# Kernel optimization log

Measured on AMD Instinct MI355X. Metric: run time of the kernel, lower is better.

Reference implementation:

```python
import jax, jax.numpy as jnp
import numpy as np

N, E, D, L, G, C = 20000, 320000, 512, 6, 64, 10
EPS = 1e-5


def setup_inputs() -> dict:
    key = jax.random.key(0)
    ks = jax.random.split(key, 8)
    s = 0.05  # small init scale to keep activations sane across 6 layers
    x = jax.random.normal(ks[0], (N, D), jnp.float32)
    edge_index = jax.random.randint(ks[1], (2, E), 0, N, jnp.int32)
    batch = jnp.sort(jax.random.randint(ks[2], (N,), 0, G, jnp.int32))
    W_rel = jax.random.normal(ks[3], (L, D, D), jnp.float32) * s
    b_rel = jnp.zeros((L, D), jnp.float32)
    W_root = jax.random.normal(ks[4], (L, D, D), jnp.float32) * s
    gamma = jnp.ones((L, D), jnp.float32)
    beta = jnp.zeros((L, D), jnp.float32)
    lin_w = jax.random.normal(ks[5], (D, C), jnp.float32) * s
    lin_b = jnp.zeros((C,), jnp.float32)
    return {"x": x, "edge_index": edge_index, "batch": batch,
            "W_rel": W_rel, "b_rel": b_rel, "W_root": W_root,
            "gamma": gamma, "beta": beta, "lin_w": lin_w, "lin_b": lin_b}


def reference(x, edge_index, batch, W_rel, b_rel, W_root, gamma, beta, lin_w, lin_b):
    # PyG GraphConv (aggr='add'): out = segment_sum(x[src] -> dst) @ W_rel + b_rel + x @ W_root
    src, dst = edge_index[0], edge_index[1]
    n = x.shape[0]
    for l in range(W_rel.shape[0]):  # 6 structurally identical layers
        agg = jax.ops.segment_sum(x[src], dst, num_segments=n)  # [N, D]
        h = agg @ W_rel[l] + b_rel[l] + x @ W_root[l]
        # BatchNorm1d in training mode: biased batch statistics over nodes
        mu = jnp.mean(h, axis=0)
        var = jnp.mean(jnp.square(h - mu), axis=0)
        x = jax.nn.relu((h - mu) * jax.lax.rsqrt(var + EPS) * gamma[l] + beta[l])
    # global_mean_pool over per-node graph ids
    sums = jax.ops.segment_sum(x, batch, num_segments=G)              # [G, D]
    counts = jax.ops.segment_sum(jnp.ones((n,), x.dtype), batch, num_segments=G)
    pooled = sums / jnp.maximum(counts, 1.0)[:, None]
    return pooled @ lin_w + lin_b  # [G, C]
```

## Files before the change

### kernel.cpp

```cpp
#include <hip/hip_runtime.h>


typedef unsigned short u16;
typedef unsigned int u32;
typedef __attribute__((ext_vector_type(8))) short bf16x8;
typedef __attribute__((ext_vector_type(16))) float f32x16;
typedef __attribute__((ext_vector_type(2))) float f32x2;

#define DFEAT 512
#define KDIM 1024
#define NLAYER 6
#define NGRAPH 64
#define NCLS 10
#define BN_EPS 1e-5f
#define NBUCKET 1024

__device__ __forceinline__ float bf_lo(u32 u) { union { u32 i; float f; } v; v.i = u << 16; return v.f; }
__device__ __forceinline__ float bf_hi(u32 u) { union { u32 i; float f; } v; v.i = u & 0xFFFF0000u; return v.f; }
__device__ __forceinline__ u16 f2bf(float f) {
  union { float f; u32 i; } v; v.f = f;
  u32 r = v.i + 0x7FFFu + ((v.i >> 16) & 1u);
  return (u16)(r >> 16);
}
__device__ __forceinline__ u32 pack2(float lo, float hi) {
  return (u32)f2bf(lo) | ((u32)f2bf(hi) << 16);
}

__device__ __forceinline__ void gload_lds16(const u16* g, u16* lds_base) {
  __builtin_amdgcn_global_load_lds(
      (const __attribute__((address_space(1))) u32*)g,
      (__attribute__((address_space(3))) u32*)lds_base, 16, 0, 0);
}

__global__ void prep_kernel(const int* __restrict__ ei, int* __restrict__ counts, int E,
                            const float* __restrict__ Wrel, const float* __restrict__ Wroot,
                            u16* __restrict__ Wt,
                            const float* __restrict__ x, u16* __restrict__ A, int M,
                            int histB, int wB) {
  __shared__ float tile[64][65];
  int b = blockIdx.x;
  int tid = threadIdx.x;
  if (b < histB) {
    int e = b * 256 + tid;
    if (e < E) atomicAdd(&counts[ei[E + e]], 1);
  } else if (b < histB + wB) {
    int t = b - histB;
    int l = t >> 7;
    int tt = t & 127;
    int k0 = (tt >> 3) << 6;
    int n0 = (tt & 7) << 6;
    int rr = tid >> 4;
    int c4 = (tid & 15) << 2;
#pragma unroll
    for (int i = 0; i < 4; i++) {
      int k = k0 + i * 16 + rr;
      const float* src = (k < DFEAT)
          ? &Wrel[((size_t)l * DFEAT + k) * DFEAT + n0 + c4]
          : &Wroot[((size_t)l * DFEAT + (k - DFEAT)) * DFEAT + n0 + c4];
      float4 v = *(const float4*)src;
      float* d = &tile[i * 16 + rr][c4];
      d[0] = v.x; d[1] = v.y; d[2] = v.z; d[3] = v.w;
    }
    __syncthreads();
    int nr = tid >> 3;
    int kc = (tid & 7) << 3;
#pragma unroll
    for (int i = 0; i < 2; i++) {
      int nl = i * 32 + nr;
      uint4 o;
      o.x = pack2(tile[kc + 0][nl], tile[kc + 1][nl]);
      o.y = pack2(tile[kc + 2][nl], tile[kc + 3][nl]);
      o.z = pack2(tile[kc + 4][nl], tile[kc + 5][nl]);
      o.w = pack2(tile[kc + 6][nl], tile[kc + 7][nl]);
      *(uint4*)&Wt[(size_t)(l * DFEAT + n0 + nl) * KDIM + k0 + kc] = o;
    }
  } else {
    int idx = (b - histB - wB) * 256 + tid;
    int row = idx >> 7;
    int c4 = (idx & 127) * 4;
    if (row < M) {
      float4 v = *(const float4*)&x[(size_t)row * DFEAT + c4];
      uint2 o; o.x = pack2(v.x, v.y); o.y = pack2(v.z, v.w);
      *(uint2*)&A[(size_t)row * KDIM + DFEAT + c4] = o;
    }
  }
}

__global__ __launch_bounds__(1024) void dscan_kernel(const int* __restrict__ counts,
                                                     int* __restrict__ base0,
                                                     int* __restrict__ bcur,
                                                     int* __restrict__ edgebase,
                                                     int* __restrict__ row_ptr2, int n) {
  __shared__ int hist[NBUCKET];
  __shared__ int part[NBUCKET];
  int tid = threadIdx.x;
  hist[tid] = 0;
  __syncthreads();
  for (int i = tid; i < n; i += 1024) {
    int d = counts[i]; if (d > NBUCKET - 1) d = NBUCKET - 1;
    atomicAdd(&hist[d], 1);
  }
  __syncthreads();
  int c = hist[tid];
  part[tid] = c; __syncthreads();
  int x = c;
  for (int off = 1; off < NBUCKET; off <<= 1) {
    int t = (tid >= off) ? part[tid - off] : 0;
    __syncthreads();
    x += t; part[tid] = x;
    __syncthreads();
  }
  base0[tid] = x - c;
  bcur[tid] = x - c;
  int w = c * tid;
  part[tid] = w; __syncthreads();
  int y = w;
  for (int off = 1; off < NBUCKET; off <<= 1) {
    int t = (tid >= off) ? part[tid - off] : 0;
    __syncthreads();
    y += t; part[tid] = y;
    __syncthreads();
  }
  edgebase[tid] = y - w;
  if (tid == NBUCKET - 1) row_ptr2[n] = y;
}

__global__ __launch_bounds__(256) void rank_kernel(const int* __restrict__ counts,
                                                   const int* __restrict__ base0,
                                                   int* __restrict__ bcur,
                                                   const int* __restrict__ edgebase,
                                                   int* __restrict__ perm,
                                                   int* __restrict__ row_ptr2,
                                                   int* __restrict__ cursor2, int n) {
  __shared__ int hb[NBUCKET];
  __shared__ int hstart[NBUCKET];
  int tid = threadIdx.x;
  for (int d = tid; d < NBUCKET; d += 256) hb[d] = 0;
  __syncthreads();
  int row = blockIdx.x * 256 + tid;
  bool valid = (row < n);
  int deg = 0, j = 0;
  if (valid) {
    deg = counts[row]; if (deg > NBUCKET - 1) deg = NBUCKET - 1;
    j = atomicAdd(&hb[deg], 1);
  }
  __syncthreads();
  for (int d = tid; d < NBUCKET; d += 256) {
    int c = hb[d];
    hstart[d] = c ? atomicAdd(&bcur[d], c) : 0;
  }
  __syncthreads();
  if (valid) {
    int rnk = hstart[deg] + j;
    int jj = rnk - base0[deg];
    int v = edgebase[deg] + jj * deg;
    perm[rnk] = row;
    row_ptr2[rnk] = v;
    cursor2[row] = v;
  }
}

__global__ void scatter_kernel(const int* __restrict__ ei, int* __restrict__ cursor2,
                               int* __restrict__ csr2, int E) {
  int e = blockIdx.x * 256 + threadIdx.x;
  if (e < E) {
    int d = ei[E + e];
    int pos = atomicAdd(&cursor2[d], 1);
    csr2[pos] = ei[e];
  }
}

template <bool FUSED>
__device__ __forceinline__ void acc8(uint4 v, const f32x2* sc, const f32x2* sh, f32x2* a) {
  f32x2 t0 = {bf_lo(v.x), bf_hi(v.x)};
  f32x2 t1 = {bf_lo(v.y), bf_hi(v.y)};
  f32x2 t2 = {bf_lo(v.z), bf_hi(v.z)};
  f32x2 t3 = {bf_lo(v.w), bf_hi(v.w)};
  if constexpr (FUSED) {
    f32x2 z = {0.f, 0.f};
    a[0] += __builtin_elementwise_max(t0 * sc[0] + sh[0], z);
    a[1] += __builtin_elementwise_max(t1 * sc[1] + sh[1], z);
    a[2] += __builtin_elementwise_max(t2 * sc[2] + sh[2], z);
    a[3] += __builtin_elementwise_max(t3 * sc[3] + sh[3], z);
  } else {
    a[0] += t0; a[1] += t1; a[2] += t2; a[3] += t3;
  }
}

#define GCAP 1536
template <bool FUSED>
__global__ __launch_bounds__(256) void gather_kernel(u16* __restrict__ A,
                                                     const u16* __restrict__ Hb,
                                                     const float* __restrict__ sums,
                                                     const float* __restrict__ gamma,
                                                     const float* __restrict__ beta,
                                                     const int* __restrict__ row_ptr2,
                                                     const int* __restrict__ csr2,
                                                     const int* __restrict__ perm,
                                                     int n, float invN) {
  __shared__ int sidx[GCAP];
  int b = blockIdx.x;
  int slice = b & 7;
  int grp = b >> 3;
  int tid = threadIdx.x;
  int r0 = grp * 32;
  int rend = (r0 + 32 < n) ? (r0 + 32) : n;
  int wbeg = row_ptr2[r0], wend = row_ptr2[rend];
  int cnt = wend - wbeg;
  bool lds_ok = (cnt <= GCAP);
  if (lds_ok)
    for (int t = tid; t < cnt; t += 256) sidx[t] = csr2[wbeg + t];
  __syncthreads();

  int wid = tid >> 6, lane = tid & 63;
  int dsub = lane >> 3, fl = lane & 7;
  int rnk = r0 + wid * 8 + dsub;
  if (rnk >= n) return;
  int dst = perm[rnk];
  int cc = slice * 64 + fl * 8;
  f32x2 sc2[4], sh2[4];
  if constexpr (FUSED) {
#pragma unroll
    for (int j = 0; j < 8; j++) {
      int c = cc + j;
      float mu = sums[c] * invN;
      float var = sums[DFEAT + c] * invN - mu * mu;
      float s = gamma[c] * rsqrtf(var + BN_EPS);
      sc2[j >> 1][j & 1] = s;
      sh2[j >> 1][j & 1] = beta[c] - mu * s;
    }
    uint4 h = *(const uint4*)&Hb[(size_t)dst * DFEAT + cc];
    f32x2 z = {0.f, 0.f};
    f32x2 e0 = __builtin_elementwise_max((f32x2){bf_lo(h.x), bf_hi(h.x)} * sc2[0] + sh2[0], z);
    f32x2 e1 = __builtin_elementwise_max((f32x2){bf_lo(h.y), bf_hi(h.y)} * sc2[1] + sh2[1], z);
    f32x2 e2 = __builtin_elementwise_max((f32x2){bf_lo(h.z), bf_hi(h.z)} * sc2[2] + sh2[2], z);
    f32x2 e3 = __builtin_elementwise_max((f32x2){bf_lo(h.w), bf_hi(h.w)} * sc2[3] + sh2[3], z);
    uint4 o;
    o.x = pack2(e0[0], e0[1]); o.y = pack2(e1[0], e1[1]);
    o.z = pack2(e2[0], e2[1]); o.w = pack2(e3[0], e3[1]);
    *(uint4*)&A[(size_t)dst * KDIM + DFEAT + cc] = o;
  }
  const u16* Sx = FUSED ? (Hb + cc) : (A + DFEAT + cc);
  const size_t RS = FUSED ? DFEAT : KDIM;
  int db = row_ptr2[rnk], de = row_ptr2[rnk + 1];
  f32x2 a[4] = {};
  if (lds_ok) {
    int e = db - wbeg, ee = de - wbeg;
    for (; e + 7 < ee; e += 8) {
      int s0 = sidx[e + 0], s1 = sidx[e + 1], s2 = sidx[e + 2], s3 = sidx[e + 3];
      int s4 = sidx[e + 4], s5 = sidx[e + 5], s6 = sidx[e + 6], s7 = sidx[e + 7];
      uint4 v0 = *(const uint4*)&Sx[(size_t)s0 * RS];
      uint4 v1 = *(const uint4*)&Sx[(size_t)s1 * RS];
      uint4 v2 = *(const uint4*)&Sx[(size_t)s2 * RS];
      uint4 v3 = *(const uint4*)&Sx[(size_t)s3 * RS];
      uint4 v4 = *(const uint4*)&Sx[(size_t)s4 * RS];
      uint4 v5 = *(const uint4*)&Sx[(size_t)s5 * RS];
      uint4 v6 = *(const uint4*)&Sx[(size_t)s6 * RS];
      uint4 v7 = *(const uint4*)&Sx[(size_t)s7 * RS];
      acc8<FUSED>(v0, sc2, sh2, a); acc8<FUSED>(v1, sc2, sh2, a);
      acc8<FUSED>(v2, sc2, sh2, a); acc8<FUSED>(v3, sc2, sh2, a);
      acc8<FUSED>(v4, sc2, sh2, a); acc8<FUSED>(v5, sc2, sh2, a);
      acc8<FUSED>(v6, sc2, sh2, a); acc8<FUSED>(v7, sc2, sh2, a);
    }
    for (; e < ee; ++e) {
      uint4 v = *(const uint4*)&Sx[(size_t)sidx[e] * RS];
      acc8<FUSED>(v, sc2, sh2, a);
    }
  } else {
    for (int e = db; e < de; ++e) {
      uint4 v = *(const uint4*)&Sx[(size_t)csr2[e] * RS];
      acc8<FUSED>(v, sc2, sh2, a);
    }
  }
  uint4 o;
  o.x = pack2(a[0][0], a[0][1]); o.y = pack2(a[1][0], a[1][1]);
  o.z = pack2(a[2][0], a[2][1]); o.w = pack2(a[3][0], a[3][1]);
  *(uint4*)&A[(size_t)dst * KDIM + cc] = o;
}

#define BM 128
#define BN 128
#define BK 64
#define CSTR 132
__global__ __launch_bounds__(256, 4) void gemm_kernel(const u16* __restrict__ A,
                                                      const u16* __restrict__ Bt,
                                                      const float* __restrict__ bias,
                                                      u16* __restrict__ Hb,
                                                      float* __restrict__ sums, int M) {
  const int lin = blockIdx.x;
  const int bx = ((lin >> 5) << 3) + (lin & 7);
  const int by = (lin >> 3) & 3;
  const int m0 = bx * BM;
  if (m0 >= M) return;
  const int n0 = by * BN;

  __shared__ u16 smem[BM * CSTR];
  __shared__ float sred[2 * BN];
  u16* As = smem;
  u16* Bs = smem + BM * BK;
  const int tid = threadIdx.x;
  const int wid = tid >> 6, lane = tid & 63;
  const int wm = wid >> 1, wn = wid & 1;
  const int l31 = lane & 31, half = lane >> 5;

  if (tid < 2 * BN) sred[tid] = 0.f;

  const int dr = lane >> 3;
  const int gcol = ((lane & 7) ^ dr) * 8;
  int arow[4], brow[4];
#pragma unroll
  for (int t = 0; t < 4; t++) {
    int r = wid * 32 + t * 8 + dr;
    int ar = m0 + r; if (ar >= M) ar = M - 1;
    arow[t] = ar;
    brow[t] = n0 + r;
  }

  f32x16 acc[2][2] = {};

  for (int k0 = 0; k0 < KDIM; k0 += BK) {
    __syncthreads();
#pragma unroll
    for (int t = 0; t < 4; t++)
      gload_lds16(&A[(size_t)arow[t] * KDIM + k0 + gcol], &As[(wid * 32 + t * 8) * BK]);
#pragma unroll
    for (int t = 0; t < 4; t++)
      gload_lds16(&Bt[(size_t)brow[t] * KDIM + k0 + gcol], &Bs[(wid * 32 + t * 8) * BK]);
    __syncthreads();
#pragma unroll
    for (int ks = 0; ks < 4; ks++) {
      int slot = ((ks * 2 + half) ^ (l31 & 7)) * 8;
      bf16x8 a0 = *(const bf16x8*)&As[(wm * 64 + l31) * BK + slot];
      bf16x8 a1 = *(const bf16x8*)&As[(wm * 64 + 32 + l31) * BK + slot];
      bf16x8 b0 = *(const bf16x8*)&Bs[(wn * 64 + l31) * BK + slot];
      bf16x8 b1 = *(const bf16x8*)&Bs[(wn * 64 + 32 + l31) * BK + slot];
      acc[0][0] = __builtin_amdgcn_mfma_f32_32x32x16_bf16(a0, b0, acc[0][0], 0, 0, 0);
      acc[0][1] = __builtin_amdgcn_mfma_f32_32x32x16_bf16(a0, b1, acc[0][1], 0, 0, 0);
      acc[1][0] = __builtin_amdgcn_mfma_f32_32x32x16_bf16(a1, b0, acc[1][0], 0, 0, 0);
      acc[1][1] = __builtin_amdgcn_mfma_f32_32x32x16_bf16(a1, b1, acc[1][1], 0, 0, 0);
    }
  }

  __syncthreads();

#pragma unroll
  for (int nt = 0; nt < 2; nt++) {
    int colt = wn * 64 + nt * 32 + l31;
    float bv = bias[n0 + colt];
    float s = 0.f, s2 = 0.f;
#pragma unroll
    for (int mt = 0; mt < 2; mt++) {
      int rbase = wm * 64 + mt * 32 + half * 4;
#pragma unroll
      for (int reg = 0; reg < 16; reg++) {
        int rowt = rbase + (reg & 3) + 8 * (reg >> 2);
        float v = acc[mt][nt][reg] + bv;
        smem[rowt * CSTR + colt] = f2bf(v);
        if (m0 + rowt < M) { s += v; s2 += v * v; }
      }
    }
    s  += __shfl_xor(s, 32);
    s2 += __shfl_xor(s2, 32);
    if (half == 0) {
      atomicAdd(&sred[colt], s);
      atomicAdd(&sred[BN + colt], s2);
    }
  }
  __syncthreads();

  const int rsub = tid >> 4;
  const int c8 = (tid & 15) * 8;
#pragma unroll
  for (int it = 0; it < 8; it++) {
    int rowt = it * 16 + rsub;
    int grow = m0 + rowt;
    if (grow < M) {
      uint4 v = *(const uint4*)&smem[rowt * CSTR + c8];
      *(uint4*)&Hb[(size_t)grow * DFEAT + n0 + c8] = v;
    }
  }
  if (tid < BN) {
    atomicAdd(&sums[n0 + tid], sred[tid]);
    atomicAdd(&sums[DFEAT + n0 + tid], sred[BN + tid]);
  }
}

__device__ __forceinline__ int lower_bound_dev(const int* a, int n, int v) {
  int lo = 0, hi = n;
  while (lo < hi) { int mid = (lo + hi) >> 1; if (a[mid] < v) lo = mid + 1; else hi = mid; }
  return lo;
}

__global__ __launch_bounds__(1024) void pool_kernel(const u16* __restrict__ Hb,
                                                    const float* __restrict__ sums,
                                                    const float* __restrict__ gamma,
                                                    const float* __restrict__ beta,
                                                    const int* __restrict__ batch,
                                                    float* __restrict__ pooled, int n, float invN) {
  __shared__ float red[DFEAT];
  int g = blockIdx.x;
  int tid = threadIdx.x;
  if (tid < DFEAT) red[tid] = 0.f;
  int lo = lower_bound_dev(batch, n, g);
  int hi = lower_bound_dev(batch, n, g + 1);
  int rowOff = tid >> 6, lane = tid & 63;
  int c0 = lane * 8;
  float sc[8], sh[8];
#pragma unroll
  for (int j = 0; j < 8; j++) {
    int c = c0 + j;
    float mu = sums[c] * invN;
    float var = sums[DFEAT + c] * invN - mu * mu;
    float s = gamma[c] * rsqrtf(var + BN_EPS);
    sc[j] = s;
    sh[j] = beta[c] - mu * s;
  }
  float a[8] = {};
  for (int r = lo + rowOff; r < hi; r += 16) {
    uint4 v = *(const uint4*)&Hb[(size_t)r * DFEAT + c0];
    float e0 = bf_lo(v.x), e1 = bf_hi(v.x), e2 = bf_lo(v.y), e3 = bf_hi(v.y);
    float e4 = bf_lo(v.z), e5 = bf_hi(v.z), e6 = bf_lo(v.w), e7 = bf_hi(v.w);
    a[0] += fmaxf(e0 * sc[0] + sh[0], 0.f); a[1] += fmaxf(e1 * sc[1] + sh[1], 0.f);
    a[2] += fmaxf(e2 * sc[2] + sh[2], 0.f); a[3] += fmaxf(e3 * sc[3] + sh[3], 0.f);
    a[4] += fmaxf(e4 * sc[4] + sh[4], 0.f); a[5] += fmaxf(e5 * sc[5] + sh[5], 0.f);
    a[6] += fmaxf(e6 * sc[6] + sh[6], 0.f); a[7] += fmaxf(e7 * sc[7] + sh[7], 0.f);
  }
  __syncthreads();
#pragma unroll
  for (int j = 0; j < 8; j++) atomicAdd(&red[c0 + j], a[j]);
  __syncthreads();
  if (tid < DFEAT) pooled[g * DFEAT + tid] = red[tid] / fmaxf((float)(hi - lo), 1.0f);
}

__global__ __launch_bounds__(64) void final_kernel(const float* __restrict__ pooled,
                                                   const float* __restrict__ lin_w,
                                                   const float* __restrict__ lin_b,
                                                   float* __restrict__ out) {
  int g = blockIdx.x;
  int lane = threadIdx.x;
  float acc[NCLS] = {};
  float4 p0 = *(const float4*)&pooled[g * DFEAT + lane * 8];
  float4 p1 = *(const float4*)&pooled[g * DFEAT + lane * 8 + 4];
  float pv[8] = {p0.x, p0.y, p0.z, p0.w, p1.x, p1.y, p1.z, p1.w};
#pragma unroll
  for (int j = 0; j < 8; j++) {
    int k = lane * 8 + j;
#pragma unroll
    for (int c = 0; c < NCLS; c++) acc[c] += pv[j] * lin_w[k * NCLS + c];
  }
#pragma unroll
  for (int off = 32; off > 0; off >>= 1)
#pragma unroll
    for (int c = 0; c < NCLS; c++) acc[c] += __shfl_down(acc[c], off);
  if (lane == 0)
#pragma unroll
    for (int c = 0; c < NCLS; c++) out[g * NCLS + c] = acc[c] + lin_b[c];
}

extern "C" void kernel_launch(void* const* d_in, const int* in_sizes, int n_in,
                              void* d_out, int out_size, void* d_ws, size_t ws_size,
                              hipStream_t stream) {
  const float* x      = (const float*)d_in[0];
  const int*   ei     = (const int*)d_in[1];
  const int*   batch  = (const int*)d_in[2];
  const float* W_rel  = (const float*)d_in[3];
  const float* b_rel  = (const float*)d_in[4];
  const float* W_root = (const float*)d_in[5];
  const float* gamma  = (const float*)d_in[6];
  const float* beta   = (const float*)d_in[7];
  const float* lin_w  = (const float*)d_in[8];
  const float* lin_b  = (const float*)d_in[9];
  float* out = (float*)d_out;

  const int N = in_sizes[0] / DFEAT;
  const int E = in_sizes[1] / 2;

  char* p = (char*)d_ws;
  u16*   A        = (u16*)p;    p += (size_t)N * KDIM * 2;
  u16*   Hb       = (u16*)p;    p += (size_t)N * DFEAT * 2;
  u16*   Wt       = (u16*)p;    p += (size_t)NLAYER * DFEAT * KDIM * 2;
  int*   row_ptr2 = (int*)p;    p += ((size_t)(N + 1) * 4 + 15) / 16 * 16;
  int*   counts   = (int*)p;    p += (size_t)N * 4;
  int*   cursor2  = (int*)p;    p += (size_t)N * 4;
  int*   perm     = (int*)p;    p += (size_t)N * 4;
  int*   csr2     = (int*)p;    p += (size_t)E * 4;
  int*   base0    = (int*)p;    p += (size_t)NBUCKET * 4;
  int*   bcur     = (int*)p;    p += (size_t)NBUCKET * 4;
  int*   edgebase = (int*)p;    p += (size_t)NBUCKET * 4;
  float* sums     = (float*)p;  p += (size_t)NLAYER * 2 * DFEAT * 4;
  float* pooled   = (float*)p;  p += (size_t)NGRAPH * DFEAT * 4;

  const float invN = 1.0f / (float)N;

  hipMemsetAsync(counts, 0, (size_t)N * 4, stream);
  hipMemsetAsync(sums, 0, (size_t)NLAYER * 2 * DFEAT * 4, stream);

  const int histB = (E + 255) / 256;
  const int wB = NLAYER * 128;
  const int xB = (N * 128 + 255) / 256;
  prep_kernel<<<histB + wB + xB, 256, 0, stream>>>(ei, counts, E, W_rel, W_root, Wt,
                                                   x, A, N, histB, wB);
  dscan_kernel<<<1, 1024, 0, stream>>>(counts, base0, bcur, edgebase, row_ptr2, N);
  rank_kernel<<<(N + 255) / 256, 256, 0, stream>>>(counts, base0, bcur, edgebase,
                                                   perm, row_ptr2, cursor2, N);
  scatter_kernel<<<(E + 255) / 256, 256, 0, stream>>>(ei, cursor2, csr2, E);

  const int ngrp8 = ((N + 31) / 32) * 8;
  const int gtiles = (((N + BM - 1) / BM + 7) / 8) * 8 * 4;

  for (int l = 0; l < NLAYER; ++l) {
    float* sums_l = sums + (size_t)l * 2 * DFEAT;
    if (l == 0)
      gather_kernel<false><<<ngrp8, 256, 0, stream>>>(A, Hb, nullptr, nullptr, nullptr,
                                                      row_ptr2, csr2, perm, N, invN);
    else
      gather_kernel<true><<<ngrp8, 256, 0, stream>>>(A, Hb,
          sums + (size_t)(l - 1) * 2 * DFEAT,
          gamma + (size_t)(l - 1) * DFEAT, beta + (size_t)(l - 1) * DFEAT,
          row_ptr2, csr2, perm, N, invN);
    gemm_kernel<<<gtiles, 256, 0, stream>>>(A, Wt + (size_t)l * DFEAT * KDIM,
                                            b_rel + (size_t)l * DFEAT, Hb, sums_l, N);
  }

  pool_kernel<<<NGRAPH, 1024, 0, stream>>>(Hb, sums + (size_t)(NLAYER - 1) * 2 * DFEAT,
                                           gamma + (size_t)(NLAYER - 1) * DFEAT,
                                           beta + (size_t)(NLAYER - 1) * DFEAT,
                                           batch, pooled, N, invN);
  final_kernel<<<NGRAPH, 64, 0, stream>>>(pooled, lin_w, lin_b, out);
}
```

Baseline: 562.3 us.

## Halve GEMM row tile, reverse gather block order, fuse classifier into pooling

The GEMM row tile drops from 128 to 64, so each wave computes a 32x64 sub-tile and the launch has twice as many blocks for the 20000-row problem. This is meant to improve load balance and occupancy across CUs, at the cost of lower per-block data reuse and more reloads of the weight tile. The gather kernel now processes row groups in reverse order, presumably so blocks with differing degree-sorted workloads are scheduled in a better order. The final linear layer is folded into the pool kernel, which removes one launch and the intermediate pooled buffer.

```diff
diff --git a/kernel.cpp b/kernel.cpp
--- a/kernel.cpp
+++ b/kernel.cpp
@@ -201,7 +201,8 @@
   __shared__ int sidx[GCAP];
   int b = blockIdx.x;
   int slice = b & 7;
-  int grp = b >> 3;
+  int nGrp = (n + 31) >> 5;
+  int grp = nGrp - 1 - (b >> 3);
   int tid = threadIdx.x;
   int r0 = grp * 32;
   int rend = (r0 + 32 < n) ? (r0 + 32) : n;
@@ -278,7 +279,7 @@
   *(uint4*)&A[(size_t)dst * KDIM + cc] = o;
 }
 
-#define BM 128
+#define BM 64
 #define BN 128
 #define BK 64
 #define CSTR 132
@@ -294,7 +295,7 @@
   if (m0 >= M) return;
   const int n0 = by * BN;
 
-  __shared__ u16 smem[BM * CSTR];
+  __shared__ u16 smem[BM * BK + BN * BK];
   __shared__ float sred[2 * BN];
   u16* As = smem;
   u16* Bs = smem + BM * BK;
@@ -307,22 +308,23 @@
 
   const int dr = lane >> 3;
   const int gcol = ((lane & 7) ^ dr) * 8;
-  int arow[4], brow[4];
-#pragma unroll
-  for (int t = 0; t < 4; t++) {
-    int r = wid * 32 + t * 8 + dr;
+  int arow[2], brow[4];
+#pragma unroll
+  for (int t = 0; t < 2; t++) {
+    int r = wid * 16 + t * 8 + dr;
     int ar = m0 + r; if (ar >= M) ar = M - 1;
     arow[t] = ar;
-    brow[t] = n0 + r;
-  }
-
-  f32x16 acc[2][2] = {};
+  }
+#pragma unroll
+  for (int t = 0; t < 4; t++) brow[t] = n0 + wid * 32 + t * 8 + dr;
+
+  f32x16 acc[2] = {};
 
   for (int k0 = 0; k0 < KDIM; k0 += BK) {
     __syncthreads();
 #pragma unroll
-    for (int t = 0; t < 4; t++)
-      gload_lds16(&A[(size_t)arow[t] * KDIM + k0 + gcol], &As[(wid * 32 + t * 8) * BK]);
+    for (int t = 0; t < 2; t++)
+      gload_lds16(&A[(size_t)arow[t] * KDIM + k0 + gcol], &As[(wid * 16 + t * 8) * BK]);
 #pragma unroll
     for (int t = 0; t < 4; t++)
       gload_lds16(&Bt[(size_t)brow[t] * KDIM + k0 + gcol], &Bs[(wid * 32 + t * 8) * BK]);
@@ -330,14 +332,11 @@
 #pragma unroll
     for (int ks = 0; ks < 4; ks++) {
       int slot = ((ks * 2 + half) ^ (l31 & 7)) * 8;
-      bf16x8 a0 = *(const bf16x8*)&As[(wm * 64 + l31) * BK + slot];
-      bf16x8 a1 = *(const bf16x8*)&As[(wm * 64 + 32 + l31) * BK + slot];
+      bf16x8 a0 = *(const bf16x8*)&As[(wm * 32 + l31) * BK + slot];
       bf16x8 b0 = *(const bf16x8*)&Bs[(wn * 64 + l31) * BK + slot];
       bf16x8 b1 = *(const bf16x8*)&Bs[(wn * 64 + 32 + l31) * BK + slot];
-      acc[0][0] = __builtin_amdgcn_mfma_f32_32x32x16_bf16(a0, b0, acc[0][0], 0, 0, 0);
-      acc[0][1] = __builtin_amdgcn_mfma_f32_32x32x16_bf16(a0, b1, acc[0][1], 0, 0, 0);
-      acc[1][0] = __builtin_amdgcn_mfma_f32_32x32x16_bf16(a1, b0, acc[1][0], 0, 0, 0);
-      acc[1][1] = __builtin_amdgcn_mfma_f32_32x32x16_bf16(a1, b1, acc[1][1], 0, 0, 0);
+      acc[0] = __builtin_amdgcn_mfma_f32_32x32x16_bf16(a0, b0, acc[0], 0, 0, 0);
+      acc[1] = __builtin_amdgcn_mfma_f32_32x32x16_bf16(a0, b1, acc[1], 0, 0, 0);
     }
   }
 
@@ -348,16 +347,13 @@
     int colt = wn * 64 + nt * 32 + l31;
     float bv = bias[n0 + colt];
     float s = 0.f, s2 = 0.f;
-#pragma unroll
-    for (int mt = 0; mt < 2; mt++) {
-      int rbase = wm * 64 + mt * 32 + half * 4;
-#pragma unroll
-      for (int reg = 0; reg < 16; reg++) {
-        int rowt = rbase + (reg & 3) + 8 * (reg >> 2);
-        float v = acc[mt][nt][reg] + bv;
-        smem[rowt * CSTR + colt] = f2bf(v);
-        if (m0 + rowt < M) { s += v; s2 += v * v; }
-      }
+    int rbase = wm * 32 + half * 4;
+#pragma unroll
+    for (int reg = 0; reg < 16; reg++) {
+      int rowt = rbase + (reg & 3) + 8 * (reg >> 2);
+      float v = acc[nt][reg] + bv;
+      smem[rowt * CSTR + colt] = f2bf(v);
+      if (m0 + rowt < M) { s += v; s2 += v * v; }
     }
     s  += __shfl_xor(s, 32);
     s2 += __shfl_xor(s2, 32);
@@ -371,7 +367,7 @@
   const int rsub = tid >> 4;
   const int c8 = (tid & 15) * 8;
 #pragma unroll
-  for (int it = 0; it < 8; it++) {
+  for (int it = 0; it < 4; it++) {
     int rowt = it * 16 + rsub;
     int grow = m0 + rowt;
     if (grow < M) {
@@ -396,11 +392,15 @@
                                                     const float* __restrict__ gamma,
                                                     const float* __restrict__ beta,
                                                     const int* __restrict__ batch,
-                                                    float* __restrict__ pooled, int n, float invN) {
+                                                    const float* __restrict__ lin_w,
+                                                    const float* __restrict__ lin_b,
+                                                    float* __restrict__ out, int n, float invN) {
   __shared__ float red[DFEAT];
+  __shared__ float outc[NCLS];
   int g = blockIdx.x;
   int tid = threadIdx.x;
   if (tid < DFEAT) red[tid] = 0.f;
+  if (tid >= DFEAT && tid < DFEAT + NCLS) outc[tid - DFEAT] = 0.f;
   int lo = lower_bound_dev(batch, n, g);
   int hi = lower_bound_dev(batch, n, g + 1);
   int rowOff = tid >> 6, lane = tid & 63;
@@ -429,32 +429,22 @@
 #pragma unroll
   for (int j = 0; j < 8; j++) atomicAdd(&red[c0 + j], a[j]);
   __syncthreads();
-  if (tid < DFEAT) pooled[g * DFEAT + tid] = red[tid] / fmaxf((float)(hi - lo), 1.0f);
-}
-
-__global__ __launch_bounds__(64) void final_kernel(const float* __restrict__ pooled,
-                                                   const float* __restrict__ lin_w,
-                                                   const float* __restrict__ lin_b,
-                                                   float* __restrict__ out) {
-  int g = blockIdx.x;
-  int lane = threadIdx.x;
-  float acc[NCLS] = {};
-  float4 p0 = *(const float4*)&pooled[g * DFEAT + lane * 8];
-  float4 p1 = *(const float4*)&pooled[g * DFEAT + lane * 8 + 4];
-  float pv[8] = {p0.x, p0.y, p0.z, p0.w, p1.x, p1.y, p1.z, p1.w};
-#pragma unroll
-  for (int j = 0; j < 8; j++) {
-    int k = lane * 8 + j;
-#pragma unroll
-    for (int c = 0; c < NCLS; c++) acc[c] += pv[j] * lin_w[k * NCLS + c];
-  }
-#pragma unroll
-  for (int off = 32; off > 0; off >>= 1)
-#pragma unroll
-    for (int c = 0; c < NCLS; c++) acc[c] += __shfl_down(acc[c], off);
-  if (lane == 0)
-#pragma unroll
-    for (int c = 0; c < NCLS; c++) out[g * NCLS + c] = acc[c] + lin_b[c];
+  float invCnt = 1.0f / fmaxf((float)(hi - lo), 1.0f);
+  if (tid < DFEAT) {
+    float pv = red[tid] * invCnt;
+    float pc[NCLS];
+#pragma unroll
+    for (int c = 0; c < NCLS; c++) pc[c] = pv * lin_w[tid * NCLS + c];
+#pragma unroll
+    for (int off = 32; off > 0; off >>= 1)
+#pragma unroll
+      for (int c = 0; c < NCLS; c++) pc[c] += __shfl_down(pc[c], off);
+    if ((tid & 63) == 0)
+#pragma unroll
+      for (int c = 0; c < NCLS; c++) atomicAdd(&outc[c], pc[c]);
+  }
+  __syncthreads();
+  if (tid < NCLS) out[g * NCLS + tid] = outc[tid] + lin_b[tid];
 }
 
 extern "C" void kernel_launch(void* const* d_in, const int* in_sizes, int n_in,
@@ -488,7 +478,6 @@
   int*   bcur     = (int*)p;    p += (size_t)NBUCKET * 4;
   int*   edgebase = (int*)p;    p += (size_t)NBUCKET * 4;
   float* sums     = (float*)p;  p += (size_t)NLAYER * 2 * DFEAT * 4;
-  float* pooled   = (float*)p;  p += (size_t)NGRAPH * DFEAT * 4;
 
   const float invN = 1.0f / (float)N;
 
@@ -525,6 +514,5 @@
   pool_kernel<<<NGRAPH, 1024, 0, stream>>>(Hb, sums + (size_t)(NLAYER - 1) * 2 * DFEAT,
                                            gamma + (size_t)(NLAYER - 1) * DFEAT,
                                            beta + (size_t)(NLAYER - 1) * DFEAT,
-                                           batch, pooled, N, invN);
-  final_kernel<<<NGRAPH, 64, 0, stream>>>(pooled, lin_w, lin_b, out);
-}
+                                           batch, lin_w, lin_b, out, N, invN);
+}
```

Measured after the change: 589.6 us. 1.05x slower.
